# Optimization experiments

Measured on AMD Instinct MI355X. Metric: run time of the kernel, lower is better.

## Reference

```python
import jax, jax.numpy as jnp
import numpy as np

BATCH, D, N = 16, 128, 16
E = N * (N - 1) // 2  # 120 candidate edges (strict upper triangle)


def _incidence(A, n):
    """Build edge-incidence matrices G, H of shape [b, n, E] from binary edge
    vector A [b, E] over the strict upper triangle of an n x n adjacency."""
    r, c = np.triu_indices(n, k=1)
    mask = (A > 0).astype(jnp.float32)  # [b, E]
    node = jnp.arange(n)[:, None]       # [n, 1]
    G = (node == jnp.asarray(r)[None, :]).astype(jnp.float32)[None] * mask[:, None, :]
    H = (node == jnp.asarray(c)[None, :]).astype(jnp.float32)[None] * mask[:, None, :]
    return G, H


def _kron(t1, t2):
    """Batched Kronecker product: t1 [b,r1,c1], t2 [b,r2,c2] -> [b,r1*r2,c1*c2]."""
    b, r1, c1 = t1.shape
    _, r2, c2 = t2.shape
    return (t1[:, :, None, :, None] * t2[:, None, :, None, :]).reshape(b, r1 * r2, c1 * c2)


def setup_inputs() -> dict:
    key = jax.random.key(0)
    ks = jax.random.split(key, 8)
    A_src = jax.random.randint(ks[0], (BATCH, E), 0, 2, dtype=jnp.int32)
    A_tgt = jax.random.randint(ks[1], (BATCH, E), 0, 2, dtype=jnp.int32)
    F_src = jax.random.normal(ks[2], (BATCH, D, N), dtype=jnp.float32)
    F_tgt = jax.random.normal(ks[3], (BATCH, D, N), dtype=jnp.float32)
    U_src = jax.random.normal(ks[4], (BATCH, N, N), dtype=jnp.float32)
    U_tgt = jax.random.normal(ks[5], (BATCH, N, N), dtype=jnp.float32)
    stdv = 1.0 / np.sqrt(D * 2)
    eye_half = jnp.eye(D, dtype=jnp.float32) / 2.0
    lambda1 = jax.random.uniform(ks[6], (D, D), jnp.float32, -stdv, stdv) + eye_half
    lambda2 = jax.random.uniform(ks[7], (D, D), jnp.float32, -stdv, stdv) + eye_half
    return {"A_src": A_src, "A_tgt": A_tgt, "F_src": F_src, "F_tgt": F_tgt,
            "U_src": U_src, "U_tgt": U_tgt, "lambda1": lambda1, "lambda2": lambda2}


def reference(A_src, A_tgt, F_src, F_tgt, U_src, U_tgt, lambda1, lambda2):
    b = F_src.shape[0]
    n, m = F_src.shape[-1], F_tgt.shape[-1]
    # symmetrized, relu'd block weight (w1 = w2 = 1)
    l1 = jax.nn.relu(lambda1 + lambda1.T)
    l2 = jax.nn.relu(lambda2 + lambda2.T)
    weight = jnp.block([[l1, l2], [l2, l1]])  # [2d, 2d]
    # incidence matrices (vectorized replacement of the per-batch scatter loop)
    G1, H1 = _incidence(A_src, n)  # [b, n, E]
    G2, H2 = _incidence(A_tgt, m)  # [b, m, E]
    # edge features: X = cat(F G, F H) -> [b, 2d, E]
    X = jnp.concatenate([F_src @ G1, F_src @ H1], axis=1)
    Y = jnp.concatenate([F_tgt @ G2, F_tgt @ H2], axis=1)
    # edge affinity M_e = X^T W Y : [b, E, E]
    M_e = jnp.einsum('bie,ij,bjf->bef', X, weight, Y)
    # node affinity M_p = U_src^T U_tgt : [b, n, m]
    M_p = jnp.einsum('bdn,bdm->bnm', U_src, U_tgt)
    K1 = _kron(G2, G1)  # [b, m*n, E*E]
    K2 = _kron(H2, H1)  # [b, m*n, E*E]
    # per-column scaling of K1 by flattened M_e (replaces per-column loop)
    K1_new = K1 * M_e.reshape(b, 1, -1)
    diagMp = jax.vmap(jnp.diag)(M_p.reshape(b, -1))  # [b, n*m, n*m]
    M = diagMp + jnp.einsum('bik,bjk->bij', K1_new, K2)
    return M
```

## Files before the change

### kernel.cpp

```cpp
#include <hip/hip_runtime.h>


#define LS 132
#define TS 17

__device__ __forceinline__ int edge_idx(int a, int p) {
    return (a * (31 - a)) / 2 + (p - a - 1);
}

__global__ __launch_bounds__(256) void kA(
    const float* __restrict__ Ftgt,
    const float* __restrict__ lam1, const float* __restrict__ lam2,
    float* __restrict__ ws)
{
    __shared__ float sRow1[16 * LS], sCol1[16 * LS];
    __shared__ float sRow2[16 * LS], sCol2[16 * LS];
    __shared__ float sFt[2048];

    const int blk = blockIdx.x;
    const int b   = blk >> 3;
    const int i0  = (blk & 7) << 4;
    const int t   = threadIdx.x;

    {
        const float4* r1 = (const float4*)(lam1 + i0 * 128);
        const float4* r2 = (const float4*)(lam2 + i0 * 128);
#pragma unroll
        for (int it = 0; it < 2; ++it) {
            const int k = t + it * 256;
            const int il = k >> 5, j4 = k & 31;
            *(float4*)(&sRow1[il * LS + j4 * 4]) = r1[il * 32 + j4];
            *(float4*)(&sRow2[il * LS + j4 * 4]) = r2[il * 32 + j4];
        }
#pragma unroll
        for (int it = 0; it < 8; ++it) {
            const int k = t + it * 256;
            const int il = k & 15, j = k >> 4;
            sCol1[il * LS + j] = lam1[j * 128 + i0 + il];
            sCol2[il * LS + j] = lam2[j * 128 + i0 + il];
        }
        const float4* f = (const float4*)(Ftgt + b * 2048);
        ((float4*)sFt)[t] = f[t];
        ((float4*)sFt)[t + 256] = f[t + 256];
    }
    __syncthreads();

    const int il = t >> 4, v = t & 15;
    float a1 = 0.f, a2 = 0.f;
#pragma unroll 8
    for (int j = 0; j < 128; ++j) {
        const float w1 = fmaxf(sRow1[il * LS + j] + sCol1[il * LS + j], 0.f);
        const float w2 = fmaxf(sRow2[il * LS + j] + sCol2[il * LS + j], 0.f);
        const float fv = sFt[(j << 4) | v];
        a1 = fmaf(w1, fv, a1);
        a2 = fmaf(w2, fv, a2);
    }
    const int i = i0 + il;
    ws[((b * 2 + 0) * 128 + i) * 16 + v] = a1;
    ws[((b * 2 + 1) * 128 + i) * 16 + v] = a2;
}

__global__ __launch_bounds__(256) void kB(
    const int* __restrict__ Asrc, const int* __restrict__ Atgt,
    const float* __restrict__ Fsrc,
    const float* __restrict__ Usrc, const float* __restrict__ Utgt,
    const float* __restrict__ ws, float* __restrict__ out)
{
    __shared__ float sT1[2048], sT2[2048], sFs[2048];
    __shared__ float sU[512];
    __shared__ float sP1[16 * TS], sP2[16 * TS], sMp[256];
    __shared__ int   smask[120];

    const int blk = blockIdx.x;
    const int b   = blk >> 4;
    const int a   = blk & 15;
    const int t   = threadIdx.x;

    {
        const float4* T1g = (const float4*)(ws + (b * 2 + 0) * 2048);
        const float4* T2g = (const float4*)(ws + (b * 2 + 1) * 2048);
        const float4* Fg  = (const float4*)(Fsrc + b * 2048);
        ((float4*)sT1)[t] = T1g[t];  ((float4*)sT1)[t + 256] = T1g[t + 256];
        ((float4*)sT2)[t] = T2g[t];  ((float4*)sT2)[t + 256] = T2g[t + 256];
        ((float4*)sFs)[t] = Fg[t];   ((float4*)sFs)[t + 256] = Fg[t + 256];
        if (t < 64)       ((float4*)sU)[t]      = ((const float4*)(Usrc + b * 256))[t];
        else if (t < 128) ((float4*)sU)[t]      = ((const float4*)(Utgt + b * 256))[t - 64];
        if (t < 120) smask[t] = (Asrc[b * 120 + t] > 0) && (Atgt[b * 120 + t] > 0);
    }
    __syncthreads();

    {
        const int u = t >> 4, v = t & 15;
        float p1 = 0.f, p2 = 0.f;
#pragma unroll 8
        for (int d = 0; d < 128; ++d) {
            const float fs = sFs[(d << 4) | u];
            p1 = fmaf(fs, sT1[(d << 4) | v], p1);
            p2 = fmaf(fs, sT2[(d << 4) | v], p2);
        }
        float mp = 0.f;
#pragma unroll
        for (int d = 0; d < 16; ++d)
            mp = fmaf(sU[(d << 4) | u], sU[256 + ((d << 4) | v)], mp);
        sP1[u * TS + v] = p1;
        sP2[u * TS + v] = p2;
        sMp[t] = mp;
    }
    __syncthreads();

    const int j0 = (t & 63) << 2;
    const int p  = j0 >> 4;
    const bool condA = (a < p) && (smask[edge_idx(a, p)] != 0);
    float* outR = out + ((size_t)b << 16) + (a << 12);
#pragma unroll
    for (int rr = 0; rr < 4; ++rr) {
        const int c = (t >> 6) + (rr << 2);
        const int r = (a << 4) | c;
        const float cpart = sP1[a * TS + c] + sP2[p * TS + c];
        float4 vec;
        float* vv = (float*)&vec;
#pragma unroll
        for (int s = 0; s < 4; ++s) {
            const int j = j0 + s, q = j & 15;
            float x = 0.f;
            if (condA && (c < q) && (smask[edge_idx(c, q)] != 0))
                x = cpart + sP2[a * TS + q] + sP1[p * TS + q];
            if (r == j) x += sMp[r];
            vv[s] = x;
        }
        *(float4*)(outR + (c << 8) + j0) = vec;
    }
}

extern "C" void kernel_launch(void* const* d_in, const int* in_sizes, int n_in,
                              void* d_out, int out_size, void* d_ws, size_t ws_size,
                              hipStream_t stream) {
    const int*   A_src = (const int*)d_in[0];
    const int*   A_tgt = (const int*)d_in[1];
    const float* F_src = (const float*)d_in[2];
    const float* F_tgt = (const float*)d_in[3];
    const float* U_src = (const float*)d_in[4];
    const float* U_tgt = (const float*)d_in[5];
    const float* lam1  = (const float*)d_in[6];
    const float* lam2  = (const float*)d_in[7];
    float* out = (float*)d_out;
    float* ws  = (float*)d_ws;

    kA<<<128, 256, 0, stream>>>(F_tgt, lam1, lam2, ws);
    kB<<<256, 256, 0, stream>>>(A_src, A_tgt, F_src, U_src, U_tgt, ws, out);
}
```

Measured before the change: 80.14 us.

## Fuse weight-projection kernel into output kernel, reassociating the bilinear product

Merges the two launches into one kernel so no workspace round-trip or second launch is needed. Each block now computes S = F_src^T W (chunked over lambda rows, with the symmetrized relu weight built in shared memory), then contracts with F_tgt, instead of reading a precomputed W·F_tgt. Each of the 256 blocks redundantly recomputes the full 16x128x128 projection for its batch, where the old kA spread it over 128 blocks. Shared memory use also grows substantially, which may reduce occupancy.

```diff
diff --git a/kernel.cpp b/kernel.cpp
--- a/kernel.cpp
+++ b/kernel.cpp
@@ -3,70 +3,25 @@
 
 #define LS 132
 #define TS 17
+#define CH 32
 
 __device__ __forceinline__ int edge_idx(int a, int p) {
     return (a * (31 - a)) / 2 + (p - a - 1);
 }
 
-__global__ __launch_bounds__(256) void kA(
-    const float* __restrict__ Ftgt,
+__global__ __launch_bounds__(256) void kOne(
+    const int* __restrict__ Asrc, const int* __restrict__ Atgt,
+    const float* __restrict__ Fsrc, const float* __restrict__ Ftgt,
+    const float* __restrict__ Usrc, const float* __restrict__ Utgt,
     const float* __restrict__ lam1, const float* __restrict__ lam2,
-    float* __restrict__ ws)
+    float* __restrict__ out)
 {
-    __shared__ float sRow1[16 * LS], sCol1[16 * LS];
-    __shared__ float sRow2[16 * LS], sCol2[16 * LS];
-    __shared__ float sFt[2048];
-
-    const int blk = blockIdx.x;
-    const int b   = blk >> 3;
-    const int i0  = (blk & 7) << 4;
-    const int t   = threadIdx.x;
-
-    {
-        const float4* r1 = (const float4*)(lam1 + i0 * 128);
-        const float4* r2 = (const float4*)(lam2 + i0 * 128);
-#pragma unroll
-        for (int it = 0; it < 2; ++it) {
-            const int k = t + it * 256;
-            const int il = k >> 5, j4 = k & 31;
-            *(float4*)(&sRow1[il * LS + j4 * 4]) = r1[il * 32 + j4];
-            *(float4*)(&sRow2[il * LS + j4 * 4]) = r2[il * 32 + j4];
-        }
-#pragma unroll
-        for (int it = 0; it < 8; ++it) {
-            const int k = t + it * 256;
-            const int il = k & 15, j = k >> 4;
-            sCol1[il * LS + j] = lam1[j * 128 + i0 + il];
-            sCol2[il * LS + j] = lam2[j * 128 + i0 + il];
-        }
-        const float4* f = (const float4*)(Ftgt + b * 2048);
-        ((float4*)sFt)[t] = f[t];
-        ((float4*)sFt)[t + 256] = f[t + 256];
-    }
-    __syncthreads();
-
-    const int il = t >> 4, v = t & 15;
-    float a1 = 0.f, a2 = 0.f;
-#pragma unroll 8
-    for (int j = 0; j < 128; ++j) {
-        const float w1 = fmaxf(sRow1[il * LS + j] + sCol1[il * LS + j], 0.f);
-        const float w2 = fmaxf(sRow2[il * LS + j] + sCol2[il * LS + j], 0.f);
-        const float fv = sFt[(j << 4) | v];
-        a1 = fmaf(w1, fv, a1);
-        a2 = fmaf(w2, fv, a2);
-    }
-    const int i = i0 + il;
-    ws[((b * 2 + 0) * 128 + i) * 16 + v] = a1;
-    ws[((b * 2 + 1) * 128 + i) * 16 + v] = a2;
-}
-
-__global__ __launch_bounds__(256) void kB(
-    const int* __restrict__ Asrc, const int* __restrict__ Atgt,
-    const float* __restrict__ Fsrc,
-    const float* __restrict__ Usrc, const float* __restrict__ Utgt,
-    const float* __restrict__ ws, float* __restrict__ out)
-{
-    __shared__ float sT1[2048], sT2[2048], sFs[2048];
+    __shared__ float sRow1[CH * LS], sCol1[CH * LS];
+    __shared__ float sRow2[CH * LS], sCol2[CH * LS];
+    __shared__ float sW1[CH * LS], sW2[CH * LS];
+    __shared__ float sFsT[16 * LS];
+    __shared__ float sFtT[16 * LS];
+    __shared__ float sS1[16 * LS], sS2[16 * LS];
     __shared__ float sU[512];
     __shared__ float sP1[16 * TS], sP2[16 * TS], sMp[256];
     __shared__ int   smask[120];
@@ -77,39 +32,122 @@
     const int t   = threadIdx.x;
 
     {
-        const float4* T1g = (const float4*)(ws + (b * 2 + 0) * 2048);
-        const float4* T2g = (const float4*)(ws + (b * 2 + 1) * 2048);
-        const float4* Fg  = (const float4*)(Fsrc + b * 2048);
-        ((float4*)sT1)[t] = T1g[t];  ((float4*)sT1)[t + 256] = T1g[t + 256];
-        ((float4*)sT2)[t] = T2g[t];  ((float4*)sT2)[t + 256] = T2g[t + 256];
-        ((float4*)sFs)[t] = Fg[t];   ((float4*)sFs)[t + 256] = Fg[t + 256];
-        if (t < 64)       ((float4*)sU)[t]      = ((const float4*)(Usrc + b * 256))[t];
-        else if (t < 128) ((float4*)sU)[t]      = ((const float4*)(Utgt + b * 256))[t - 64];
+        const float4* fsp = (const float4*)(Fsrc + b * 2048);
+        const float4* ftp = (const float4*)(Ftgt + b * 2048);
+#pragma unroll
+        for (int it = 0; it < 2; ++it) {
+            const int k = t + it * 256;
+            const int d = k >> 2, x0 = (k & 3) * 4;
+            const float4 f = fsp[k];
+            sFsT[(x0 + 0) * LS + d] = f.x;
+            sFsT[(x0 + 1) * LS + d] = f.y;
+            sFsT[(x0 + 2) * LS + d] = f.z;
+            sFsT[(x0 + 3) * LS + d] = f.w;
+            const float4 g = ftp[k];
+            sFtT[(x0 + 0) * LS + d] = g.x;
+            sFtT[(x0 + 1) * LS + d] = g.y;
+            sFtT[(x0 + 2) * LS + d] = g.z;
+            sFtT[(x0 + 3) * LS + d] = g.w;
+        }
+        if (t < 64)       ((float4*)sU)[t] = ((const float4*)(Usrc + b * 256))[t];
+        else if (t < 128) ((float4*)sU)[t] = ((const float4*)(Utgt + b * 256))[t - 64];
         if (t < 120) smask[t] = (Asrc[b * 120 + t] > 0) && (Atgt[b * 120 + t] > 0);
     }
+
+    const int u  = t >> 4;
+    const int jg = t & 15;
+    float acc1[8], acc2[8];
+#pragma unroll
+    for (int s = 0; s < 8; ++s) { acc1[s] = 0.f; acc2[s] = 0.f; }
+
+    for (int i0 = 0; i0 < 128; i0 += CH) {
+        const float4* r1 = (const float4*)(lam1 + i0 * 128);
+        const float4* r2 = (const float4*)(lam2 + i0 * 128);
+#pragma unroll
+        for (int it = 0; it < 4; ++it) {
+            const int k = t + it * 256;
+            const int il = k >> 5, j4 = k & 31;
+            *(float4*)(&sRow1[il * LS + j4 * 4]) = r1[il * 32 + j4];
+            *(float4*)(&sRow2[il * LS + j4 * 4]) = r2[il * 32 + j4];
+        }
+#pragma unroll
+        for (int it = 0; it < 16; ++it) {
+            const int k = t + it * 256;
+            const int il = k & 31, j = k >> 5;
+            sCol1[il * LS + j] = lam1[j * 128 + i0 + il];
+            sCol2[il * LS + j] = lam2[j * 128 + i0 + il];
+        }
+        __syncthreads();
+
+#pragma unroll
+        for (int g = 0; g < 4; ++g) {
+            const int k = t + g * 256;
+            const int il = k >> 5, j4 = (k & 31) * 4;
+            const float4 r = *(const float4*)(&sRow1[il * LS + j4]);
+            const float4 c = *(const float4*)(&sCol1[il * LS + j4]);
+            float4 w;
+            w.x = fmaxf(r.x + c.x, 0.f);  w.y = fmaxf(r.y + c.y, 0.f);
+            w.z = fmaxf(r.z + c.z, 0.f);  w.w = fmaxf(r.w + c.w, 0.f);
+            *(float4*)(&sW1[il * LS + j4]) = w;
+            const float4 r2v = *(const float4*)(&sRow2[il * LS + j4]);
+            const float4 c2v = *(const float4*)(&sCol2[il * LS + j4]);
+            float4 w2;
+            w2.x = fmaxf(r2v.x + c2v.x, 0.f);  w2.y = fmaxf(r2v.y + c2v.y, 0.f);
+            w2.z = fmaxf(r2v.z + c2v.z, 0.f);  w2.w = fmaxf(r2v.w + c2v.w, 0.f);
+            *(float4*)(&sW2[il * LS + j4]) = w2;
+        }
+        __syncthreads();
+
+#pragma unroll 8
+        for (int il = 0; il < CH; ++il) {
+            const float f1 = sFsT[u * LS + i0 + il];
+            const float4 wA = *(const float4*)(&sW1[il * LS + jg * 4]);
+            const float4 wB = *(const float4*)(&sW1[il * LS + 64 + jg * 4]);
+            acc1[0] = fmaf(f1, wA.x, acc1[0]);  acc1[1] = fmaf(f1, wA.y, acc1[1]);
+            acc1[2] = fmaf(f1, wA.z, acc1[2]);  acc1[3] = fmaf(f1, wA.w, acc1[3]);
+            acc1[4] = fmaf(f1, wB.x, acc1[4]);  acc1[5] = fmaf(f1, wB.y, acc1[5]);
+            acc1[6] = fmaf(f1, wB.z, acc1[6]);  acc1[7] = fmaf(f1, wB.w, acc1[7]);
+            const float4 vA = *(const float4*)(&sW2[il * LS + jg * 4]);
+            const float4 vB = *(const float4*)(&sW2[il * LS + 64 + jg * 4]);
+            acc2[0] = fmaf(f1, vA.x, acc2[0]);  acc2[1] = fmaf(f1, vA.y, acc2[1]);
+            acc2[2] = fmaf(f1, vA.z, acc2[2]);  acc2[3] = fmaf(f1, vA.w, acc2[3]);
+            acc2[4] = fmaf(f1, vB.x, acc2[4]);  acc2[5] = fmaf(f1, vB.y, acc2[5]);
+            acc2[6] = fmaf(f1, vB.z, acc2[6]);  acc2[7] = fmaf(f1, vB.w, acc2[7]);
+        }
+        __syncthreads();
+    }
+
+    *(float4*)(&sS1[u * LS + jg * 4])      = make_float4(acc1[0], acc1[1], acc1[2], acc1[3]);
+    *(float4*)(&sS1[u * LS + 64 + jg * 4]) = make_float4(acc1[4], acc1[5], acc1[6], acc1[7]);
+    *(float4*)(&sS2[u * LS + jg * 4])      = make_float4(acc2[0], acc2[1], acc2[2], acc2[3]);
+    *(float4*)(&sS2[u * LS + 64 + jg * 4]) = make_float4(acc2[4], acc2[5], acc2[6], acc2[7]);
     __syncthreads();
 
     {
-        const int u = t >> 4, v = t & 15;
+        const int u2 = t >> 4, v = t & 15;
         float p1 = 0.f, p2 = 0.f;
 #pragma unroll 8
-        for (int d = 0; d < 128; ++d) {
-            const float fs = sFs[(d << 4) | u];
-            p1 = fmaf(fs, sT1[(d << 4) | v], p1);
-            p2 = fmaf(fs, sT2[(d << 4) | v], p2);
+        for (int j0 = 0; j0 < 128; j0 += 4) {
+            const float4 ft = *(const float4*)(&sFtT[v * LS + j0]);
+            const float4 s1 = *(const float4*)(&sS1[u2 * LS + j0]);
+            const float4 s2 = *(const float4*)(&sS2[u2 * LS + j0]);
+            p1 = fmaf(s1.x, ft.x, p1);  p2 = fmaf(s2.x, ft.x, p2);
+            p1 = fmaf(s1.y, ft.y, p1);  p2 = fmaf(s2.y, ft.y, p2);
+            p1 = fmaf(s1.z, ft.z, p1);  p2 = fmaf(s2.z, ft.z, p2);
+            p1 = fmaf(s1.w, ft.w, p1);  p2 = fmaf(s2.w, ft.w, p2);
         }
         float mp = 0.f;
 #pragma unroll
         for (int d = 0; d < 16; ++d)
-            mp = fmaf(sU[(d << 4) | u], sU[256 + ((d << 4) | v)], mp);
-        sP1[u * TS + v] = p1;
-        sP2[u * TS + v] = p2;
+            mp = fmaf(sU[(d << 4) | u2], sU[256 + ((d << 4) | v)], mp);
+        sP1[u2 * TS + v] = p1;
+        sP2[u2 * TS + v] = p2;
         sMp[t] = mp;
     }
     __syncthreads();
 
-    const int j0 = (t & 63) << 2;
-    const int p  = j0 >> 4;
+    const int j0c = (t & 63) << 2;
+    const int p   = j0c >> 4;
     const bool condA = (a < p) && (smask[edge_idx(a, p)] != 0);
     float* outR = out + ((size_t)b << 16) + (a << 12);
 #pragma unroll
@@ -121,14 +159,14 @@
         float* vv = (float*)&vec;
 #pragma unroll
         for (int s = 0; s < 4; ++s) {
-            const int j = j0 + s, q = j & 15;
+            const int j = j0c + s, q = j & 15;
             float x = 0.f;
             if (condA && (c < q) && (smask[edge_idx(c, q)] != 0))
                 x = cpart + sP2[a * TS + q] + sP1[p * TS + q];
             if (r == j) x += sMp[r];
             vv[s] = x;
         }
-        *(float4*)(outR + (c << 8) + j0) = vec;
+        *(float4*)(outR + (c << 8) + j0c) = vec;
     }
 }
 
@@ -144,8 +182,7 @@
     const float* lam1  = (const float*)d_in[6];
     const float* lam2  = (const float*)d_in[7];
     float* out = (float*)d_out;
-    float* ws  = (float*)d_ws;
 
-    kA<<<128, 256, 0, stream>>>(F_tgt, lam1, lam2, ws);
-    kB<<<256, 256, 0, stream>>>(A_src, A_tgt, F_src, U_src, U_tgt, ws, out);
+    kOne<<<256, 256, 0, stream>>>(A_src, A_tgt, F_src, F_tgt,
+                                  U_src, U_tgt, lam1, lam2, out);
 }
```

Result: slower. 85.63 us (+6.8%).
